# Optimization experiments

Hardware: AMD Instinct MI355X
Metric: run time of the kernel (lower is better)

The kernel has to match this reference:

```python
import jax, jax.numpy as jnp
import numpy as np

B, L, D, H = 256, 256, 128, 256
IMPUTE_WEIGHT = 1.0


def setup_inputs() -> dict:
    key = jax.random.key(0)
    ks = jax.random.split(key, 20)
    s = 0.05
    inp = {
        "values": jax.random.normal(ks[0], (B, L, D), jnp.float32),
        "masks": jax.random.randint(ks[1], (B, L, D), 0, 2).astype(jnp.float32),
        "deltas": jax.random.uniform(ks[2], (B, L, D), jnp.float32),
        "eval_masks": jax.random.randint(ks[3], (B, L, D), 0, 2).astype(jnp.float32),
        "td_h_W": jax.random.normal(ks[4], (H, D), jnp.float32) * s,
        "td_h_b": jax.random.normal(ks[5], (H,), jnp.float32) * s,
        "td_x_w": jax.random.normal(ks[6], (D,), jnp.float32) * s,  # diag of TemporalDecay(diag=True)
        "td_x_b": jax.random.normal(ks[7], (D,), jnp.float32) * s,
        "hist_W": jax.random.normal(ks[8], (D, H), jnp.float32) * s,
        "hist_b": jax.random.normal(ks[9], (D,), jnp.float32) * s,
        "feat_W": jax.random.normal(ks[10], (D, D), jnp.float32) * s,
        "feat_b": jax.random.normal(ks[11], (D,), jnp.float32) * s,
        "wc_W": jax.random.normal(ks[12], (D, 2 * D), jnp.float32) * s,
        "wc_b": jax.random.normal(ks[13], (D,), jnp.float32) * s,
        "W_ih": jax.random.normal(ks[14], (4 * H, 2 * D), jnp.float32) * s,
        "W_hh": jax.random.normal(ks[15], (4 * H, H), jnp.float32) * s,
        "b_ih": jax.random.normal(ks[16], (4 * H,), jnp.float32) * s,
        "b_hh": jax.random.normal(ks[17], (4 * H,), jnp.float32) * s,
    }
    return inp


def _rits_forward(values, masks, deltas, eval_masks,
                  td_h_W, td_h_b, td_x_w, td_x_b,
                  hist_W, hist_b, feat_W, feat_b,
                  wc_W, wc_b, W_ih, W_hh, b_ih, b_hh):
    feat_mask = 1.0 - jnp.eye(D, dtype=values.dtype)  # zero diagonal
    Wf = feat_W * feat_mask

    def step(carry, xs):
        h, c, loss = carry
        x, m, d, me = xs  # each (B, D)
        gamma_h = jnp.exp(-jax.nn.relu(d @ td_h_W.T + td_h_b))   # (B, H)
        gamma_x = jnp.exp(-jax.nn.relu(d * td_x_w + td_x_b))      # (B, D) diag linear
        h = h * gamma_h
        x_h = h @ hist_W.T + hist_b                               # (B, D)
        x_c = m * x + (1.0 - m) * x_h
        z_h = x_c @ Wf.T + feat_b                                 # (B, D)
        alpha = jnp.concatenate([gamma_x, m], axis=1) @ wc_W.T + wc_b
        c_h = alpha * z_h + (1.0 - alpha) * x_h
        c_c = m * x + (1.0 - m) * c_h
        loss = loss + jnp.sum(jnp.abs(c_c - x) * me) / (jnp.sum(me) + 1e-5)
        inputs = jnp.concatenate([c_c, m], axis=1)                # (B, 2D)
        gates = inputs @ W_ih.T + b_ih + h @ W_hh.T + b_hh        # (B, 4H)
        i, f, g, o = jnp.split(gates, 4, axis=1)
        i, f, o = jax.nn.sigmoid(i), jax.nn.sigmoid(f), jax.nn.sigmoid(o)
        g = jnp.tanh(g)
        c = f * c + i * g
        h = o * jnp.tanh(c)
        return (h, c, loss), c_c

    h0 = jnp.zeros((values.shape[0], H), values.dtype)
    c0 = jnp.zeros((values.shape[0], H), values.dtype)
    loss0 = jnp.zeros((), values.dtype)
    xs = (jnp.swapaxes(values, 0, 1), jnp.swapaxes(masks, 0, 1),
          jnp.swapaxes(deltas, 0, 1), jnp.swapaxes(eval_masks, 0, 1))  # (L, B, D)
    (_, _, loss), imps = jax.lax.scan(step, (h0, c0, loss0), xs)
    imputations = jnp.swapaxes(imps, 0, 1)  # (B, L, D)
    return imputations, loss * IMPUTE_WEIGHT


def reference(values, masks, deltas, eval_masks,
              td_h_W, td_h_b, td_x_w, td_x_b,
              hist_W, hist_b, feat_W, feat_b,
              wc_W, wc_b, W_ih, W_hh, b_ih, b_hh):
    return _rits_forward(values, masks, deltas, eval_masks,
                         td_h_W, td_h_b, td_x_w, td_x_b,
                         hist_W, hist_b, feat_W, feat_b,
                         wc_W, wc_b, W_ih, W_hh, b_ih, b_hh)
```

## Files before the change

### kernel.cpp

```cpp
#include <hip/hip_runtime.h>
#include <math.h>


namespace {
constexpr int Bn = 256, Ln = 256, Dn = 128, Hn = 256;
constexpr long LD = (long)Ln * Dn;

constexpr int OFF_LOSS  = 0;
constexpr int OFF_DEN   = 256;
constexpr int OFF_BIASG = 2048;
constexpr int OFF_WG    = 8192;
constexpr int OFF_HISTP = 1056768;
constexpr int OFF_TDHP  = 1122304;
constexpr int OFF_WFP   = 1187840;
constexpr int OFF_WCP   = 1220608;
constexpr int OFF_EXCH  = 1286144;
constexpr int OFF_FLAG  = 1810432;
}

typedef _Float16 h2f __attribute__((ext_vector_type(2)));
typedef unsigned int uint32;

__device__ __forceinline__ float fdot2(uint32 a, uint32 b, float c) {
  return __builtin_amdgcn_fdot2(__builtin_bit_cast(h2f, a),
                                __builtin_bit_cast(h2f, b), c, false);
}
__device__ __forceinline__ uint32 packf16(float a, float b) {
  h2f p; p[0] = (_Float16)a; p[1] = (_Float16)b;
  return __builtin_bit_cast(uint32, p);
}

__global__ void rits_prep(const float* __restrict__ td_h_W,
                          const float* __restrict__ hist_W,
                          const float* __restrict__ feat_W,
                          const float* __restrict__ wc_W,
                          const float* __restrict__ W_ih,
                          const float* __restrict__ W_hh,
                          const float* __restrict__ b_ih,
                          const float* __restrict__ b_hh,
                          const float* __restrict__ evalm,
                          char* __restrict__ wsb) {
  const int blk = blockIdx.x, tid = threadIdx.x;
  if (blk < 1248) {
    int idx = blk * 256 + tid;
    if (idx < 262144) {
      int kp = idx >> 11, rem = idx & 2047, jj = rem >> 3, s8 = rem & 7;
      const float* src = (s8 < 4) ? W_ih : W_hh;
      int q = s8 & 3;
      const float* row = src + (size_t)(q * 256 + jj) * 256 + 2 * kp;
      ((uint32*)(wsb + OFF_WG))[idx] = packf16(row[0], row[1]);
    } else if (idx < 278528) {
      int i2 = idx - 262144, kp = i2 >> 7, d = i2 & 127;
      ((uint32*)(wsb + OFF_HISTP))[i2] =
          packf16(hist_W[d * 256 + 2 * kp], hist_W[d * 256 + 2 * kp + 1]);
    } else if (idx < 294912) {
      int i2 = idx - 278528, kp = i2 >> 8, h = i2 & 255;
      ((uint32*)(wsb + OFF_TDHP))[i2] =
          packf16(td_h_W[h * 128 + 2 * kp], td_h_W[h * 128 + 2 * kp + 1]);
    } else if (idx < 303104) {
      int i2 = idx - 294912, kp = i2 >> 7, d = i2 & 127;
      float a = (2 * kp == d) ? 0.f : feat_W[d * 128 + 2 * kp];
      float b = (2 * kp + 1 == d) ? 0.f : feat_W[d * 128 + 2 * kp + 1];
      ((uint32*)(wsb + OFF_WFP))[i2] = packf16(a, b);
    } else if (idx < 319488) {
      int i2 = idx - 303104, kp = i2 >> 7, d = i2 & 127;
      ((uint32*)(wsb + OFF_WCP))[i2] =
          packf16(wc_W[d * 256 + 2 * kp], wc_W[d * 256 + 2 * kp + 1]);
    }
  } else if (blk < 1252) {
    int i = (blk - 1248) * 256 + tid;
    int jj = i >> 2, q = i & 3;
    ((float*)(wsb + OFF_BIASG))[jj * 4 + q] =
        b_ih[q * 256 + jj] + b_hh[q * 256 + jj];
    if (blk == 1248 && tid == 0) *((float*)(wsb + OFF_LOSS)) = 0.f;
  } else if (blk < 1508) {
    int t = blk - 1252;
    __shared__ float red[256];
    int d = tid & 127, g = tid >> 7;
    float s = 0.f;
    for (int b = g; b < 256; b += 2) s += evalm[(size_t)b * LD + t * 128 + d];
    red[tid] = s;
    __syncthreads();
    for (int o = 128; o > 0; o >>= 1) {
      if (tid < o) red[tid] += red[tid + o];
      __syncthreads();
    }
    if (tid == 0) ((float*)(wsb + OFF_DEN))[t] = red[0] + 1e-5f;
  } else {
    for (int i = tid; i < 4096; i += 256) ((uint32*)(wsb + OFF_FLAG))[i] = 0u;
  }
}

__global__ __launch_bounds__(512, 2) void rits_rec(
    const float* __restrict__ values, const float* __restrict__ masks,
    const float* __restrict__ deltas, const float* __restrict__ evalm,
    const float* __restrict__ td_h_b, const float* __restrict__ td_x_w,
    const float* __restrict__ td_x_b, const float* __restrict__ hist_b,
    const float* __restrict__ feat_b, const float* __restrict__ wc_b,
    char* __restrict__ wsb, float* __restrict__ outp) {
  __shared__ uint32 histL[16384];
  __shared__ uint32 wfL[8192];
  __shared__ __align__(16) float scratch[4608];
  __shared__ float al_s[4][128];
  __shared__ float hf[4][64], cst[4][64];
  __shared__ __align__(16) uint32 hdP[512];
  __shared__ __align__(16) uint32 cmP[512];
  __shared__ __align__(16) uint32 xcP[256];
  __shared__ __align__(16) uint32 drP[256];
  __shared__ __align__(16) uint32 gxmP[512];
  __shared__ float bg_s[256];
  __shared__ float tdhb_s[64];
  __shared__ float txw_s[128], txb_s[128], hb_s[128], fb_s[128], wcb_s[128];

  const int tid = threadIdx.x;
  const int bid = blockIdx.x;
  const int sh = bid >> 6;
  const int grp = bid & 63;
  const size_t b0 = (size_t)grp * 4;
  const uint32* wg = (const uint32*)(wsb + OFF_WG);
  const uint32* tdhG = (const uint32*)(wsb + OFF_TDHP);
  const uint32* wcG = (const uint32*)(wsb + OFF_WCP);
  const float* denG = (const float*)(wsb + OFF_DEN);
  char* exch = wsb + OFF_EXCH;
  unsigned int* flg = (unsigned int*)(wsb + OFF_FLAG);

  {
    const uint4* hG = (const uint4*)(wsb + OFF_HISTP);
#pragma unroll
    for (int k = 0; k < 8; ++k) ((uint4*)histL)[k * 512 + tid] = hG[k * 512 + tid];
    const uint4* fG = (const uint4*)(wsb + OFF_WFP);
#pragma unroll
    for (int k = 0; k < 4; ++k) ((uint4*)wfL)[k * 512 + tid] = fG[k * 512 + tid];
  }
  if (tid < 256) {
    bg_s[tid] = ((const float*)(wsb + OFF_BIASG))[(sh * 64 + (tid & 63)) * 4 + (tid >> 6)];
  } else if (tid < 320) tdhb_s[tid - 256] = td_h_b[sh * 64 + (tid - 256)];
  else if (tid < 448) txw_s[tid - 320] = td_x_w[tid - 320];
  if (tid < 128) txb_s[tid] = td_x_b[tid];
  else if (tid < 256) hb_s[tid - 128] = hist_b[tid - 128];
  else if (tid < 384) fb_s[tid - 256] = feat_b[tid - 256];
  else wcb_s[tid - 384] = wc_b[tid - 384];
  if (tid < 256) ((float*)hf)[tid] = 0.f;
  else ((float*)cst)[tid - 256] = 0.f;

  const int dA = tid & 127, rA = tid >> 7;
  const int hlB = tid & 63, kqB = (tid >> 6) & 7;
  const int dlB = tid & 31, kqA = tid >> 5;
  const int jjH = tid & 63, qhH = (tid >> 6) & 1, kqH = tid >> 7;
  const int jg = sh * 64 + jjH;

  uint2 wv_[32], wh_[32];
#pragma unroll
  for (int i = 0; i < 32; ++i) {
    const uint32* p = wg + ((size_t)((kqH * 32 + i) * 256 + jg)) * 8 + 2 * qhH;
    wv_[i] = *(const uint2*)p;
    wh_[i] = *(const uint2*)(p + 4);
  }
  uint32 tw[8];
#pragma unroll
  for (int i = 0; i < 8; ++i) tw[i] = tdhG[(kqB * 8 + i) * 256 + sh * 64 + hlB];
  uint32 cw[8];
#pragma unroll
  for (int i = 0; i < 8; ++i) cw[i] = wcG[(kqA * 8 + i) * 128 + sh * 32 + dlB];
  __syncthreads();

  float lacc = 0.f;
  for (int t = 0; t < Ln; ++t) {
    const size_t base = b0 * LD + (size_t)t * 128;
    uint32* mypU = (uint32*)(exch + (size_t)(bid * 2 + (t & 1)) * 1024);

    const size_t gi = base + (size_t)rA * LD + dA;
    const float xv = values[gi];
    const float mv = masks[gi];
    const float ev = evalm[gi];
    {
      const size_t gb = base + (size_t)rA * LD;
      if (dA < 64) {
        float d0v = deltas[gb + 2 * dA], d1v = deltas[gb + 2 * dA + 1];
        drP[dA * 4 + rA] = packf16(d0v, d1v);
        float g0 = __expf(-fmaxf(fmaf(d0v, txw_s[2 * dA], txb_s[2 * dA]), 0.f));
        float g1 = __expf(-fmaxf(fmaf(d1v, txw_s[2 * dA + 1], txb_s[2 * dA + 1]), 0.f));
        gxmP[dA * 4 + rA] = packf16(g0, g1);
      } else {
        int k2 = dA - 64;
        gxmP[dA * 4 + rA] = packf16(masks[gb + 2 * k2], masks[gb + 2 * k2 + 1]);
      }
    }
    __syncthreads();

    {
      float ga0 = 0.f, ga1 = 0.f, ga2 = 0.f, ga3 = 0.f;
#pragma unroll
      for (int i = 0; i < 8; ++i) {
        uint4 d4 = *(const uint4*)&drP[(kqB * 8 + i) * 4];
        ga0 = fdot2(d4.x, tw[i], ga0); ga1 = fdot2(d4.y, tw[i], ga1);
        ga2 = fdot2(d4.z, tw[i], ga2); ga3 = fdot2(d4.w, tw[i], ga3);
      }
      scratch[2304 + (kqB * 4 + 0) * 68 + hlB] = ga0;
      scratch[2304 + (kqB * 4 + 1) * 68 + hlB] = ga1;
      scratch[2304 + (kqB * 4 + 2) * 68 + hlB] = ga2;
      scratch[2304 + (kqB * 4 + 3) * 68 + hlB] = ga3;
      float aa0 = 0.f, aa1 = 0.f, aa2 = 0.f, aa3 = 0.f;
#pragma unroll
      for (int i = 0; i < 8; ++i) {
        uint4 g4 = *(const uint4*)&gxmP[(kqA * 8 + i) * 4];
        aa0 = fdot2(g4.x, cw[i], aa0); aa1 = fdot2(g4.y, cw[i], aa1);
        aa2 = fdot2(g4.z, cw[i], aa2); aa3 = fdot2(g4.w, cw[i], aa3);
      }
      scratch[(kqA * 4 + 0) * 36 + dlB] = aa0;
      scratch[(kqA * 4 + 1) * 36 + dlB] = aa1;
      scratch[(kqA * 4 + 2) * 36 + dlB] = aa2;
      scratch[(kqA * 4 + 3) * 36 + dlB] = aa3;
    }
    __syncthreads();

    if (tid < 256) {
      int hl = tid & 63, r = tid >> 6;
      float s = tdhb_s[hl];
#pragma unroll
      for (int kq = 0; kq < 8; ++kq) s += scratch[2304 + (kq * 4 + r) * 68 + hl];
      float hd = hf[r][hl] * __expf(-fmaxf(s, 0.f));
      float hdo = __shfl_down(hd, 1);
      if (!(hl & 1)) {
        uint32 pv = packf16(hd, hdo);
        int kpl = hl >> 1;
        hdP[(sh * 32 + kpl) * 4 + r] = pv;
        __hip_atomic_store(mypU + kpl * 4 + r, pv, __ATOMIC_RELAXED,
                           __HIP_MEMORY_SCOPE_AGENT);
      }
    } else if (tid < 384) {
      int i0 = tid - 256, dl = i0 & 31, r = i0 >> 5;
      float s = wcb_s[sh * 32 + dl];
#pragma unroll
      for (int kq = 0; kq < 16; ++kq) s += scratch[(kq * 4 + r) * 36 + dl];
      al_s[r][sh * 32 + dl] = s;
      __hip_atomic_store(mypU + 128 + r * 32 + dl,
                         __builtin_bit_cast(uint32, s),
                         __ATOMIC_RELAXED, __HIP_MEMORY_SCOPE_AGENT);
    }
    __syncthreads();

    if (tid == 0)
      __hip_atomic_store(flg + bid * 16, (unsigned)(t + 1), __ATOMIC_RELEASE,
                         __HIP_MEMORY_SCOPE_AGENT);
    if (tid < 3) {
      int ps = tid + (tid >= sh ? 1 : 0);
      unsigned* pfp = flg + (ps * 64 + grp) * 16;
      unsigned guard = 0;
      while (__hip_atomic_load(pfp, __ATOMIC_ACQUIRE,
                               __HIP_MEMORY_SCOPE_AGENT) < (unsigned)(t + 1)) {
        if (++guard > (1u << 24)) break;
      }
    }
    __syncthreads();

    if (tid < 256) {
#pragma unroll
      for (int p = 0; p < 3; ++p) {
        int ps = p + (p >= sh ? 1 : 0);
        const uint32* pq =
            (const uint32*)(exch + (size_t)((ps * 64 + grp) * 2 + (t & 1)) * 1024);
        uint32 v = __hip_atomic_load(pq + tid, __ATOMIC_RELAXED,
                                     __HIP_MEMORY_SCOPE_AGENT);
        if (tid < 128) hdP[ps * 128 + tid] = v;
        else {
          int i = tid - 128;
          al_s[i >> 5][ps * 32 + (i & 31)] = __builtin_bit_cast(float, v);
        }
      }
    }
    __syncthreads();

    float xhv;
    {
      float xh = hb_s[dA];
#pragma unroll 16
      for (int kp = 0; kp < 128; ++kp)
        xh = fdot2(hdP[kp * 4 + rA], histL[kp * 128 + dA], xh);
      xhv = xh;
      float xc = mv * xv + (1.f - mv) * xh;
      float xco = __shfl_down(xc, 1);
      if (!(dA & 1)) xcP[((dA >> 1)) * 4 + rA] = packf16(xc, xco);
    }
    __syncthreads();

    {
      float z = fb_s[dA];
#pragma unroll 16
      for (int kp = 0; kp < 64; ++kp)
        z = fdot2(xcP[kp * 4 + rA], wfL[kp * 128 + dA], z);
      float a = al_s[rA][dA];
      float ch = a * z + (1.f - a) * xhv;
      float cc = mv * xv + (1.f - mv) * ch;
      if (rA == sh) {
        outp[base + (size_t)rA * LD + dA] = cc;
        lacc += (1.f - mv) * fabsf(ch - xv) * ev / denG[t];
      }
      float cco = __shfl_down(cc, 1);
      float mmo = __shfl_down(mv, 1);
      if (!(dA & 1)) {
        cmP[(dA >> 1) * 4 + rA] = packf16(cc, cco);
        cmP[(64 + (dA >> 1)) * 4 + rA] = packf16(mv, mmo);
      }
    }
    __syncthreads();

    {
      float a00 = 0.f, a01 = 0.f, a02 = 0.f, a03 = 0.f;
      float a10 = 0.f, a11 = 0.f, a12 = 0.f, a13 = 0.f;
#pragma unroll
      for (int i = 0; i < 32; ++i) {
        int kp = kqH * 32 + i;
        uint4 c4 = *(const uint4*)&cmP[kp * 4];
        uint4 h4 = *(const uint4*)&hdP[kp * 4];
        a00 = fdot2(c4.x, wv_[i].x, a00); a10 = fdot2(c4.x, wv_[i].y, a10);
        a00 = fdot2(h4.x, wh_[i].x, a00); a10 = fdot2(h4.x, wh_[i].y, a10);
        a01 = fdot2(c4.y, wv_[i].x, a01); a11 = fdot2(c4.y, wv_[i].y, a11);
        a01 = fdot2(h4.y, wh_[i].x, a01); a11 = fdot2(h4.y, wh_[i].y, a11);
        a02 = fdot2(c4.z, wv_[i].x, a02); a12 = fdot2(c4.z, wv_[i].y, a12);
        a02 = fdot2(h4.z, wh_[i].x, a02); a12 = fdot2(h4.z, wh_[i].y, a12);
        a03 = fdot2(c4.w, wv_[i].x, a03); a13 = fdot2(c4.w, wv_[i].y, a13);
        a03 = fdot2(h4.w, wh_[i].x, a03); a13 = fdot2(h4.w, wh_[i].y, a13);
      }
      const int q0 = 2 * qhH, q1 = 2 * qhH + 1;
      scratch[(kqH * 16 + 0 * 4 + q0) * 64 + jjH] = a00;
      scratch[(kqH * 16 + 1 * 4 + q0) * 64 + jjH] = a01;
      scratch[(kqH * 16 + 2 * 4 + q0) * 64 + jjH] = a02;
      scratch[(kqH * 16 + 3 * 4 + q0) * 64 + jjH] = a03;
      scratch[(kqH * 16 + 0 * 4 + q1) * 64 + jjH] = a10;
      scratch[(kqH * 16 + 1 * 4 + q1) * 64 + jjH] = a11;
      scratch[(kqH * 16 + 2 * 4 + q1) * 64 + jjH] = a12;
      scratch[(kqH * 16 + 3 * 4 + q1) * 64 + jjH] = a13;
    }
    __syncthreads();

    if (tid < 256) {
      int jj = tid & 63, r = tid >> 6;
      float g0 = bg_s[0 * 64 + jj], g1 = bg_s[1 * 64 + jj];
      float g2 = bg_s[2 * 64 + jj], g3 = bg_s[3 * 64 + jj];
#pragma unroll
      for (int kq = 0; kq < 4; ++kq) {
        int bx = (kq * 16 + r * 4) * 64 + jj;
        g0 += scratch[bx]; g1 += scratch[bx + 64];
        g2 += scratch[bx + 128]; g3 += scratch[bx + 192];
      }
      float ig = 1.f / (1.f + __expf(-g0));
      float fg = 1.f / (1.f + __expf(-g1));
      float gg = tanhf(g2);
      float og = 1.f / (1.f + __expf(-g3));
      float c = fg * cst[r][jj] + ig * gg;
      cst[r][jj] = c;
      hf[r][jj] = og * tanhf(c);
    }
    __syncthreads();
  }

  scratch[tid] = lacc;
  __syncthreads();
  for (int o = 256; o > 0; o >>= 1) {
    if (tid < o) scratch[tid] += scratch[tid + o];
    __syncthreads();
  }
  if (tid == 0) atomicAdd((float*)(wsb + OFF_LOSS), scratch[0]);
}

__global__ void rits_fin(const char* __restrict__ wsb, float* __restrict__ outp) {
  if (threadIdx.x == 0 && blockIdx.x == 0)
    outp[(size_t)Bn * LD] = *((const float*)(wsb + OFF_LOSS));
}

extern "C" void kernel_launch(void* const* d_in, const int* in_sizes, int n_in,
                              void* d_out, int out_size, void* d_ws,
                              size_t ws_size, hipStream_t stream) {
  const float* values = (const float*)d_in[0];
  const float* masks  = (const float*)d_in[1];
  const float* deltas = (const float*)d_in[2];
  const float* evalm  = (const float*)d_in[3];
  const float* td_h_W = (const float*)d_in[4];
  const float* td_h_b = (const float*)d_in[5];
  const float* td_x_w = (const float*)d_in[6];
  const float* td_x_b = (const float*)d_in[7];
  const float* hist_W = (const float*)d_in[8];
  const float* hist_b = (const float*)d_in[9];
  const float* feat_W = (const float*)d_in[10];
  const float* feat_b = (const float*)d_in[11];
  const float* wc_W   = (const float*)d_in[12];
  const float* wc_b   = (const float*)d_in[13];
  const float* W_ih   = (const float*)d_in[14];
  const float* W_hh   = (const float*)d_in[15];
  const float* b_ih   = (const float*)d_in[16];
  const float* b_hh   = (const float*)d_in[17];
  char* wsb = (char*)d_ws;
  float* outp = (float*)d_out;

  hipLaunchKernelGGL(rits_prep, dim3(1509), dim3(256), 0, stream, td_h_W,
                     hist_W, feat_W, wc_W, W_ih, W_hh, b_ih, b_hh, evalm, wsb);
  hipLaunchKernelGGL(rits_rec, dim3(256), dim3(512), 0, stream, values, masks,
                     deltas, evalm, td_h_b, td_x_w, td_x_b, hist_b, feat_b,
                     wc_b, wsb, outp);
  hipLaunchKernelGGL(rits_fin, dim3(1), dim3(64), 0, stream, wsb, outp);
}
```

Before: 3.693 ms.

## Widen recurrent blocks to 1024 threads and pipeline per-step work

The recurrent kernel doubles its thread count and splits the GEMV reductions further along K. The next step's decay gamma_h is computed right after the LSTM update, and the wc projection runs while the hidden state is exchanged. Inputs for the next steps are prefetched into registers, and the flag wait is spread across waves so each polls its own peer. The imputation loss moves to a separate post-pass kernel that re-reads outputs, values and eval masks. This cuts the number of barriers on the serial critical path, at the cost of fewer waves per CU and an extra full pass over memory for the loss.

```diff
diff --git a/kernel.cpp b/kernel.cpp
--- a/kernel.cpp
+++ b/kernel.cpp
@@ -91,26 +91,25 @@
   }
 }
 
-__global__ __launch_bounds__(512, 2) void rits_rec(
+__global__ __launch_bounds__(1024, 4) void rits_rec(
     const float* __restrict__ values, const float* __restrict__ masks,
-    const float* __restrict__ deltas, const float* __restrict__ evalm,
+    const float* __restrict__ deltas,
     const float* __restrict__ td_h_b, const float* __restrict__ td_x_w,
     const float* __restrict__ td_x_b, const float* __restrict__ hist_b,
     const float* __restrict__ feat_b, const float* __restrict__ wc_b,
     char* __restrict__ wsb, float* __restrict__ outp) {
   __shared__ uint32 histL[16384];
   __shared__ uint32 wfL[8192];
-  __shared__ __align__(16) float scratch[4608];
-  __shared__ float al_s[4][128];
-  __shared__ float hf[4][64], cst[4][64];
+  __shared__ __align__(16) float scratch[9216];
   __shared__ __align__(16) uint32 hdP[512];
   __shared__ __align__(16) uint32 cmP[512];
   __shared__ __align__(16) uint32 xcP[256];
   __shared__ __align__(16) uint32 drP[256];
   __shared__ __align__(16) uint32 gxmP[512];
-  __shared__ float bg_s[256];
-  __shared__ float tdhb_s[64];
+  __shared__ float gbufF[256];
+  __shared__ float hf[4][64], cst[4][64];
   __shared__ float txw_s[128], txb_s[128], hb_s[128], fb_s[128], wcb_s[128];
+  __shared__ float tdhb_s[64], bg_s[256];
 
   const int tid = threadIdx.x;
   const int bid = blockIdx.x;
@@ -120,182 +119,184 @@
   const uint32* wg = (const uint32*)(wsb + OFF_WG);
   const uint32* tdhG = (const uint32*)(wsb + OFF_TDHP);
   const uint32* wcG = (const uint32*)(wsb + OFF_WCP);
-  const float* denG = (const float*)(wsb + OFF_DEN);
   char* exch = wsb + OFF_EXCH;
   unsigned int* flg = (unsigned int*)(wsb + OFF_FLAG);
 
+  const int dA = tid & 127, rA = tid >> 7;
+  const int dD = tid & 127, kqD = tid >> 7;
+  const int jjH = tid & 63, qhH = (tid >> 6) & 1, kqH = tid >> 7;
+  const int jg = sh * 64 + jjH;
+  const int jjG = tid & 63, rG = (tid >> 6) & 3, kslG = tid >> 8;
+
   {
     const uint4* hG = (const uint4*)(wsb + OFF_HISTP);
 #pragma unroll
-    for (int k = 0; k < 8; ++k) ((uint4*)histL)[k * 512 + tid] = hG[k * 512 + tid];
+    for (int k = 0; k < 4; ++k) ((uint4*)histL)[k * 1024 + tid] = hG[k * 1024 + tid];
     const uint4* fG = (const uint4*)(wsb + OFF_WFP);
 #pragma unroll
-    for (int k = 0; k < 4; ++k) ((uint4*)wfL)[k * 512 + tid] = fG[k * 512 + tid];
-  }
-  if (tid < 256) {
-    bg_s[tid] = ((const float*)(wsb + OFF_BIASG))[(sh * 64 + (tid & 63)) * 4 + (tid >> 6)];
-  } else if (tid < 320) tdhb_s[tid - 256] = td_h_b[sh * 64 + (tid - 256)];
-  else if (tid < 448) txw_s[tid - 320] = td_x_w[tid - 320];
-  if (tid < 128) txb_s[tid] = td_x_b[tid];
-  else if (tid < 256) hb_s[tid - 128] = hist_b[tid - 128];
-  else if (tid < 384) fb_s[tid - 256] = feat_b[tid - 256];
-  else wcb_s[tid - 384] = wc_b[tid - 384];
+    for (int k = 0; k < 2; ++k) ((uint4*)wfL)[k * 1024 + tid] = fG[k * 1024 + tid];
+  }
+  if (tid < 128) txw_s[tid] = td_x_w[tid];
+  else if (tid < 256) txb_s[tid - 128] = td_x_b[tid - 128];
+  else if (tid < 384) hb_s[tid - 256] = hist_b[tid - 256];
+  else if (tid < 512) fb_s[tid - 384] = feat_b[tid - 384];
+  else if (tid < 640) wcb_s[tid - 512] = wc_b[tid - 512];
+  else if (tid < 704) tdhb_s[tid - 640] = td_h_b[sh * 64 + (tid - 640)];
+  else if (tid < 960) {
+    int i = tid - 704;
+    bg_s[i] = ((const float*)(wsb + OFF_BIASG))[(sh * 64 + (i & 63)) * 4 + (i >> 6)];
+  }
   if (tid < 256) ((float*)hf)[tid] = 0.f;
-  else ((float*)cst)[tid - 256] = 0.f;
-
-  const int dA = tid & 127, rA = tid >> 7;
-  const int hlB = tid & 63, kqB = (tid >> 6) & 7;
-  const int dlB = tid & 31, kqA = tid >> 5;
-  const int jjH = tid & 63, qhH = (tid >> 6) & 1, kqH = tid >> 7;
-  const int jg = sh * 64 + jjH;
-
-  uint2 wv_[32], wh_[32];
-#pragma unroll
-  for (int i = 0; i < 32; ++i) {
-    const uint32* p = wg + ((size_t)((kqH * 32 + i) * 256 + jg)) * 8 + 2 * qhH;
+  else if (tid < 512) ((float*)cst)[tid - 256] = 0.f;
+
+  uint2 wv_[16], wh_[16];
+#pragma unroll
+  for (int i = 0; i < 16; ++i) {
+    const uint32* p = wg + ((size_t)((kqH * 16 + i) * 256 + jg)) * 8 + 2 * qhH;
     wv_[i] = *(const uint2*)p;
     wh_[i] = *(const uint2*)(p + 4);
   }
-  uint32 tw[8];
-#pragma unroll
-  for (int i = 0; i < 8; ++i) tw[i] = tdhG[(kqB * 8 + i) * 256 + sh * 64 + hlB];
-  uint32 cw[8];
-#pragma unroll
-  for (int i = 0; i < 8; ++i) cw[i] = wcG[(kqA * 8 + i) * 128 + sh * 32 + dlB];
+  uint32 twr[16];
+#pragma unroll
+  for (int i = 0; i < 16; ++i)
+    twr[i] = tdhG[(kslG * 16 + i) * 256 + sh * 64 + jjG];
   __syncthreads();
 
-  float lacc = 0.f;
+  float xv = 0.f, mv = 0.f, xvn = 0.f, mvn = 0.f, dvn = 0.f;
+  if (tid < 512) {
+    size_t g0 = b0 * LD + (size_t)rA * LD + dA;
+    xv = values[g0]; mv = masks[g0];
+    float dv0 = deltas[g0];
+    float gx = __expf(-fmaxf(fmaf(dv0, txw_s[dA], txb_s[dA]), 0.f));
+    float gxo = __shfl_down(gx, 1);
+    float dvo = __shfl_down(dv0, 1);
+    float mvo = __shfl_down(mv, 1);
+    if (!(dA & 1)) {
+      gxmP[(dA >> 1) * 4 + rA] = packf16(gx, gxo);
+      gxmP[(64 + (dA >> 1)) * 4 + rA] = packf16(mv, mvo);
+      drP[(dA >> 1) * 4 + rA] = packf16(dv0, dvo);
+    }
+    size_t g1 = g0 + 128;
+    xvn = values[g1]; mvn = masks[g1]; dvn = deltas[g1];
+  }
+  __syncthreads();
+  {
+    float gp = 0.f;
+#pragma unroll
+    for (int i = 0; i < 16; ++i)
+      gp = fdot2(drP[(kslG * 16 + i) * 4 + rG], twr[i], gp);
+    scratch[8192 + (kslG * 4 + rG) * 64 + jjG] = gp;
+  }
+  __syncthreads();
+  if (tid < 256) {
+    int jj = tid & 63, r = tid >> 6;
+    float s = tdhb_s[jj];
+#pragma unroll
+    for (int ks = 0; ks < 4; ++ks) s += scratch[8192 + (ks * 4 + r) * 64 + jj];
+    gbufF[r * 64 + jj] = __expf(-fmaxf(s, 0.f));
+  }
+  __syncthreads();
+
+  float xh = 0.f, av = 0.f;
   for (int t = 0; t < Ln; ++t) {
     const size_t base = b0 * LD + (size_t)t * 128;
     uint32* mypU = (uint32*)(exch + (size_t)(bid * 2 + (t & 1)) * 1024);
 
-    const size_t gi = base + (size_t)rA * LD + dA;
-    const float xv = values[gi];
-    const float mv = masks[gi];
-    const float ev = evalm[gi];
-    {
-      const size_t gb = base + (size_t)rA * LD;
-      if (dA < 64) {
-        float d0v = deltas[gb + 2 * dA], d1v = deltas[gb + 2 * dA + 1];
-        drP[dA * 4 + rA] = packf16(d0v, d1v);
-        float g0 = __expf(-fmaxf(fmaf(d0v, txw_s[2 * dA], txb_s[2 * dA]), 0.f));
-        float g1 = __expf(-fmaxf(fmaf(d1v, txw_s[2 * dA + 1], txb_s[2 * dA + 1]), 0.f));
-        gxmP[dA * 4 + rA] = packf16(g0, g1);
-      } else {
-        int k2 = dA - 64;
-        gxmP[dA * 4 + rA] = packf16(masks[gb + 2 * k2], masks[gb + 2 * k2 + 1]);
-      }
-    }
-    __syncthreads();
-
-    {
-      float ga0 = 0.f, ga1 = 0.f, ga2 = 0.f, ga3 = 0.f;
-#pragma unroll
-      for (int i = 0; i < 8; ++i) {
-        uint4 d4 = *(const uint4*)&drP[(kqB * 8 + i) * 4];
-        ga0 = fdot2(d4.x, tw[i], ga0); ga1 = fdot2(d4.y, tw[i], ga1);
-        ga2 = fdot2(d4.z, tw[i], ga2); ga3 = fdot2(d4.w, tw[i], ga3);
-      }
-      scratch[2304 + (kqB * 4 + 0) * 68 + hlB] = ga0;
-      scratch[2304 + (kqB * 4 + 1) * 68 + hlB] = ga1;
-      scratch[2304 + (kqB * 4 + 2) * 68 + hlB] = ga2;
-      scratch[2304 + (kqB * 4 + 3) * 68 + hlB] = ga3;
-      float aa0 = 0.f, aa1 = 0.f, aa2 = 0.f, aa3 = 0.f;
-#pragma unroll
-      for (int i = 0; i < 8; ++i) {
-        uint4 g4 = *(const uint4*)&gxmP[(kqA * 8 + i) * 4];
-        aa0 = fdot2(g4.x, cw[i], aa0); aa1 = fdot2(g4.y, cw[i], aa1);
-        aa2 = fdot2(g4.z, cw[i], aa2); aa3 = fdot2(g4.w, cw[i], aa3);
-      }
-      scratch[(kqA * 4 + 0) * 36 + dlB] = aa0;
-      scratch[(kqA * 4 + 1) * 36 + dlB] = aa1;
-      scratch[(kqA * 4 + 2) * 36 + dlB] = aa2;
-      scratch[(kqA * 4 + 3) * 36 + dlB] = aa3;
-    }
-    __syncthreads();
-
-    if (tid < 256) {
-      int hl = tid & 63, r = tid >> 6;
-      float s = tdhb_s[hl];
-#pragma unroll
-      for (int kq = 0; kq < 8; ++kq) s += scratch[2304 + (kq * 4 + r) * 68 + hl];
-      float hd = hf[r][hl] * __expf(-fmaxf(s, 0.f));
-      float hdo = __shfl_down(hd, 1);
-      if (!(hl & 1)) {
-        uint32 pv = packf16(hd, hdo);
-        int kpl = hl >> 1;
-        hdP[(sh * 32 + kpl) * 4 + r] = pv;
-        __hip_atomic_store(mypU + kpl * 4 + r, pv, __ATOMIC_RELAXED,
-                           __HIP_MEMORY_SCOPE_AGENT);
-      }
-    } else if (tid < 384) {
-      int i0 = tid - 256, dl = i0 & 31, r = i0 >> 5;
-      float s = wcb_s[sh * 32 + dl];
-#pragma unroll
-      for (int kq = 0; kq < 16; ++kq) s += scratch[(kq * 4 + r) * 36 + dl];
-      al_s[r][sh * 32 + dl] = s;
-      __hip_atomic_store(mypU + 128 + r * 32 + dl,
-                         __builtin_bit_cast(uint32, s),
-                         __ATOMIC_RELAXED, __HIP_MEMORY_SCOPE_AGENT);
+    if (tid < 128) {
+      int kpl = tid & 31, r = tid >> 5;
+      float g0 = gbufF[r * 64 + 2 * kpl], g1 = gbufF[r * 64 + 2 * kpl + 1];
+      uint32 pv = packf16(hf[r][2 * kpl] * g0, hf[r][2 * kpl + 1] * g1);
+      hdP[(sh * 32 + kpl) * 4 + r] = pv;
+      __hip_atomic_store(mypU + kpl * 4 + r, pv, __ATOMIC_RELAXED,
+                         __HIP_MEMORY_SCOPE_AGENT);
+    } else if (tid >= 512) {
+      int i0 = tid - 512, d = i0 & 127, kq = i0 >> 7;
+      float a0 = 0.f, a1 = 0.f, a2 = 0.f, a3 = 0.f;
+#pragma unroll 8
+      for (int i2 = 0; i2 < 32; ++i2) {
+        int kp = kq * 32 + i2;
+        uint32 w = wcG[kp * 128 + d];
+        uint4 g4 = *(const uint4*)&gxmP[kp * 4];
+        a0 = fdot2(g4.x, w, a0); a1 = fdot2(g4.y, w, a1);
+        a2 = fdot2(g4.z, w, a2); a3 = fdot2(g4.w, w, a3);
+      }
+      scratch[4096 + (kq * 4 + 0) * 128 + d] = a0;
+      scratch[4096 + (kq * 4 + 1) * 128 + d] = a1;
+      scratch[4096 + (kq * 4 + 2) * 128 + d] = a2;
+      scratch[4096 + (kq * 4 + 3) * 128 + d] = a3;
     }
     __syncthreads();
 
     if (tid == 0)
       __hip_atomic_store(flg + bid * 16, (unsigned)(t + 1), __ATOMIC_RELEASE,
                          __HIP_MEMORY_SCOPE_AGENT);
-    if (tid < 3) {
-      int ps = tid + (tid >= sh ? 1 : 0);
+    if (tid < 384) {
+      int w = tid >> 6, lane = tid & 63;
+      int p = w >> 1;
+      int ps = p + (p >= sh ? 1 : 0);
       unsigned* pfp = flg + (ps * 64 + grp) * 16;
-      unsigned guard = 0;
-      while (__hip_atomic_load(pfp, __ATOMIC_ACQUIRE,
-                               __HIP_MEMORY_SCOPE_AGENT) < (unsigned)(t + 1)) {
-        if (++guard > (1u << 24)) break;
-      }
-    }
-    __syncthreads();
-
-    if (tid < 256) {
-#pragma unroll
-      for (int p = 0; p < 3; ++p) {
-        int ps = p + (p >= sh ? 1 : 0);
-        const uint32* pq =
-            (const uint32*)(exch + (size_t)((ps * 64 + grp) * 2 + (t & 1)) * 1024);
-        uint32 v = __hip_atomic_load(pq + tid, __ATOMIC_RELAXED,
-                                     __HIP_MEMORY_SCOPE_AGENT);
-        if (tid < 128) hdP[ps * 128 + tid] = v;
-        else {
-          int i = tid - 128;
-          al_s[i >> 5][ps * 32 + (i & 31)] = __builtin_bit_cast(float, v);
+      if (lane == 0) {
+        unsigned guard = 0;
+        while (__hip_atomic_load(pfp, __ATOMIC_ACQUIRE,
+                                 __HIP_MEMORY_SCOPE_AGENT) < (unsigned)(t + 1)) {
+          if (++guard > (1u << 22)) break;
         }
       }
-    }
-    __syncthreads();
-
-    float xhv;
+      int j = ((w & 1) << 6) + lane;
+      const uint32* pq =
+          (const uint32*)(exch + (size_t)((ps * 64 + grp) * 2 + (t & 1)) * 1024);
+      hdP[ps * 128 + j] = __hip_atomic_load(pq + j, __ATOMIC_RELAXED,
+                                            __HIP_MEMORY_SCOPE_AGENT);
+    }
+    __syncthreads();
+
     {
-      float xh = hb_s[dA];
-#pragma unroll 16
-      for (int kp = 0; kp < 128; ++kp)
-        xh = fdot2(hdP[kp * 4 + rA], histL[kp * 128 + dA], xh);
-      xhv = xh;
+      float a0 = 0.f, a1 = 0.f, a2 = 0.f, a3 = 0.f;
+#pragma unroll
+      for (int i = 0; i < 16; ++i) {
+        int kp = kqD * 16 + i;
+        uint32 w = histL[kp * 128 + dD];
+        uint4 h4 = *(const uint4*)&hdP[kp * 4];
+        a0 = fdot2(h4.x, w, a0); a1 = fdot2(h4.y, w, a1);
+        a2 = fdot2(h4.z, w, a2); a3 = fdot2(h4.w, w, a3);
+      }
+      scratch[(kqD * 4 + 0) * 128 + dD] = a0;
+      scratch[(kqD * 4 + 1) * 128 + dD] = a1;
+      scratch[(kqD * 4 + 2) * 128 + dD] = a2;
+      scratch[(kqD * 4 + 3) * 128 + dD] = a3;
+    }
+    __syncthreads();
+
+    if (tid < 512) {
+      xh = hb_s[dA];
+#pragma unroll
+      for (int kq = 0; kq < 8; ++kq) xh += scratch[(kq * 4 + rA) * 128 + dA];
+      av = wcb_s[dA];
+#pragma unroll
+      for (int kq = 0; kq < 4; ++kq) av += scratch[4096 + (kq * 4 + rA) * 128 + dA];
       float xc = mv * xv + (1.f - mv) * xh;
       float xco = __shfl_down(xc, 1);
-      if (!(dA & 1)) xcP[((dA >> 1)) * 4 + rA] = packf16(xc, xco);
-    }
-    __syncthreads();
-
-    {
+      if (!(dA & 1)) xcP[(dA >> 1) * 4 + rA] = packf16(xc, xco);
+      float gx = __expf(-fmaxf(fmaf(dvn, txw_s[dA], txb_s[dA]), 0.f));
+      float gxo = __shfl_down(gx, 1);
+      float dvo = __shfl_down(dvn, 1);
+      float mvo = __shfl_down(mvn, 1);
+      if (!(dA & 1)) {
+        gxmP[(dA >> 1) * 4 + rA] = packf16(gx, gxo);
+        gxmP[(64 + (dA >> 1)) * 4 + rA] = packf16(mvn, mvo);
+        drP[(dA >> 1) * 4 + rA] = packf16(dvn, dvo);
+      }
+    }
+    __syncthreads();
+
+    if (tid < 512) {
       float z = fb_s[dA];
 #pragma unroll 16
       for (int kp = 0; kp < 64; ++kp)
         z = fdot2(xcP[kp * 4 + rA], wfL[kp * 128 + dA], z);
-      float a = al_s[rA][dA];
-      float ch = a * z + (1.f - a) * xhv;
+      float ch = av * z + (1.f - av) * xh;
       float cc = mv * xv + (1.f - mv) * ch;
-      if (rA == sh) {
-        outp[base + (size_t)rA * LD + dA] = cc;
-        lacc += (1.f - mv) * fabsf(ch - xv) * ev / denG[t];
-      }
+      if (rA == sh) outp[base + (size_t)rA * LD + dA] = cc;
       float cco = __shfl_down(cc, 1);
       float mmo = __shfl_down(mv, 1);
       if (!(dA & 1)) {
@@ -306,40 +307,46 @@
     __syncthreads();
 
     {
-      float a00 = 0.f, a01 = 0.f, a02 = 0.f, a03 = 0.f;
-      float a10 = 0.f, a11 = 0.f, a12 = 0.f, a13 = 0.f;
-#pragma unroll
-      for (int i = 0; i < 32; ++i) {
-        int kp = kqH * 32 + i;
+      float a[4][2] = {};
+#pragma unroll
+      for (int i = 0; i < 16; ++i) {
+        int kp = kqH * 16 + i;
         uint4 c4 = *(const uint4*)&cmP[kp * 4];
         uint4 h4 = *(const uint4*)&hdP[kp * 4];
-        a00 = fdot2(c4.x, wv_[i].x, a00); a10 = fdot2(c4.x, wv_[i].y, a10);
-        a00 = fdot2(h4.x, wh_[i].x, a00); a10 = fdot2(h4.x, wh_[i].y, a10);
-        a01 = fdot2(c4.y, wv_[i].x, a01); a11 = fdot2(c4.y, wv_[i].y, a11);
-        a01 = fdot2(h4.y, wh_[i].x, a01); a11 = fdot2(h4.y, wh_[i].y, a11);
-        a02 = fdot2(c4.z, wv_[i].x, a02); a12 = fdot2(c4.z, wv_[i].y, a12);
-        a02 = fdot2(h4.z, wh_[i].x, a02); a12 = fdot2(h4.z, wh_[i].y, a12);
-        a03 = fdot2(c4.w, wv_[i].x, a03); a13 = fdot2(c4.w, wv_[i].y, a13);
-        a03 = fdot2(h4.w, wh_[i].x, a03); a13 = fdot2(h4.w, wh_[i].y, a13);
-      }
-      const int q0 = 2 * qhH, q1 = 2 * qhH + 1;
-      scratch[(kqH * 16 + 0 * 4 + q0) * 64 + jjH] = a00;
-      scratch[(kqH * 16 + 1 * 4 + q0) * 64 + jjH] = a01;
-      scratch[(kqH * 16 + 2 * 4 + q0) * 64 + jjH] = a02;
-      scratch[(kqH * 16 + 3 * 4 + q0) * 64 + jjH] = a03;
-      scratch[(kqH * 16 + 0 * 4 + q1) * 64 + jjH] = a10;
-      scratch[(kqH * 16 + 1 * 4 + q1) * 64 + jjH] = a11;
-      scratch[(kqH * 16 + 2 * 4 + q1) * 64 + jjH] = a12;
-      scratch[(kqH * 16 + 3 * 4 + q1) * 64 + jjH] = a13;
-    }
-    __syncthreads();
-
+        a[0][0] = fdot2(c4.x, wv_[i].x, a[0][0]); a[0][0] = fdot2(h4.x, wh_[i].x, a[0][0]);
+        a[0][1] = fdot2(c4.x, wv_[i].y, a[0][1]); a[0][1] = fdot2(h4.x, wh_[i].y, a[0][1]);
+        a[1][0] = fdot2(c4.y, wv_[i].x, a[1][0]); a[1][0] = fdot2(h4.y, wh_[i].x, a[1][0]);
+        a[1][1] = fdot2(c4.y, wv_[i].y, a[1][1]); a[1][1] = fdot2(h4.y, wh_[i].y, a[1][1]);
+        a[2][0] = fdot2(c4.z, wv_[i].x, a[2][0]); a[2][0] = fdot2(h4.z, wh_[i].x, a[2][0]);
+        a[2][1] = fdot2(c4.z, wv_[i].y, a[2][1]); a[2][1] = fdot2(h4.z, wh_[i].y, a[2][1]);
+        a[3][0] = fdot2(c4.w, wv_[i].x, a[3][0]); a[3][0] = fdot2(h4.w, wh_[i].x, a[3][0]);
+        a[3][1] = fdot2(c4.w, wv_[i].y, a[3][1]); a[3][1] = fdot2(h4.w, wh_[i].y, a[3][1]);
+      }
+#pragma unroll
+      for (int r = 0; r < 4; ++r) {
+        scratch[(kqH * 16 + r * 4 + 2 * qhH) * 64 + jjH] = a[r][0];
+        scratch[(kqH * 16 + r * 4 + 2 * qhH + 1) * 64 + jjH] = a[r][1];
+      }
+      float gp = 0.f;
+#pragma unroll
+      for (int i = 0; i < 16; ++i)
+        gp = fdot2(drP[(kslG * 16 + i) * 4 + rG], twr[i], gp);
+      scratch[8192 + (kslG * 4 + rG) * 64 + jjG] = gp;
+    }
+    __syncthreads();
+
+    if (tid < 512) {
+      xv = xvn; mv = mvn;
+      int t2 = (t + 2) & 255;
+      size_t g2 = b0 * LD + (size_t)t2 * 128 + (size_t)rA * LD + dA;
+      xvn = values[g2]; mvn = masks[g2]; dvn = deltas[g2];
+    }
     if (tid < 256) {
       int jj = tid & 63, r = tid >> 6;
       float g0 = bg_s[0 * 64 + jj], g1 = bg_s[1 * 64 + jj];
       float g2 = bg_s[2 * 64 + jj], g3 = bg_s[3 * 64 + jj];
 #pragma unroll
-      for (int kq = 0; kq < 4; ++kq) {
+      for (int kq = 0; kq < 8; ++kq) {
         int bx = (kq * 16 + r * 4) * 64 + jj;
         g0 += scratch[bx]; g1 += scratch[bx + 64];
         g2 += scratch[bx + 128]; g3 += scratch[bx + 192];
@@ -351,20 +358,39 @@
       float c = fg * cst[r][jj] + ig * gg;
       cst[r][jj] = c;
       hf[r][jj] = og * tanhf(c);
-    }
-    __syncthreads();
-  }
-
-  scratch[tid] = lacc;
+      float s = tdhb_s[jj];
+#pragma unroll
+      for (int ks = 0; ks < 4; ++ks) s += scratch[8192 + (ks * 4 + r) * 64 + jj];
+      gbufF[r * 64 + jj] = __expf(-fmaxf(s, 0.f));
+    }
+    __syncthreads();
+  }
+}
+
+__global__ void rits_fin1(const float* __restrict__ values,
+                          const float* __restrict__ evalm,
+                          const float* __restrict__ outp,
+                          char* __restrict__ wsb) {
+  const int t = blockIdx.x, tid = threadIdx.x;
+  __shared__ float red[256];
+  int d = tid & 127, g = tid >> 7;
+  float s = 0.f;
+  for (int b = g; b < 256; b += 2) {
+    size_t ix = (size_t)b * LD + (size_t)t * 128 + d;
+    s += fabsf(outp[ix] - values[ix]) * evalm[ix];
+  }
+  red[tid] = s;
   __syncthreads();
-  for (int o = 256; o > 0; o >>= 1) {
-    if (tid < o) scratch[tid] += scratch[tid + o];
-    __syncthreads();
-  }
-  if (tid == 0) atomicAdd((float*)(wsb + OFF_LOSS), scratch[0]);
-}
-
-__global__ void rits_fin(const char* __restrict__ wsb, float* __restrict__ outp) {
+  for (int o = 128; o > 0; o >>= 1) {
+    if (tid < o) red[tid] += red[tid + o];
+    __syncthreads();
+  }
+  if (tid == 0)
+    atomicAdd((float*)(wsb + OFF_LOSS),
+              red[0] / ((const float*)(wsb + OFF_DEN))[t]);
+}
+
+__global__ void rits_fin2(const char* __restrict__ wsb, float* __restrict__ outp) {
   if (threadIdx.x == 0 && blockIdx.x == 0)
     outp[(size_t)Bn * LD] = *((const float*)(wsb + OFF_LOSS));
 }
@@ -395,8 +421,10 @@
 
   hipLaunchKernelGGL(rits_prep, dim3(1509), dim3(256), 0, stream, td_h_W,
                      hist_W, feat_W, wc_W, W_ih, W_hh, b_ih, b_hh, evalm, wsb);
-  hipLaunchKernelGGL(rits_rec, dim3(256), dim3(512), 0, stream, values, masks,
-                     deltas, evalm, td_h_b, td_x_w, td_x_b, hist_b, feat_b,
+  hipLaunchKernelGGL(rits_rec, dim3(256), dim3(1024), 0, stream, values, masks,
+                     deltas, td_h_b, td_x_w, td_x_b, hist_b, feat_b,
                      wc_b, wsb, outp);
-  hipLaunchKernelGGL(rits_fin, dim3(1), dim3(64), 0, stream, wsb, outp);
-}
+  hipLaunchKernelGGL(rits_fin1, dim3(256), dim3(256), 0, stream, values, evalm,
+                     outp, wsb);
+  hipLaunchKernelGGL(rits_fin2, dim3(1), dim3(64), 0, stream, wsb, outp);
+}
```

New measurement: 12.56 ms. 240% more time.
